# Optimization experiments

Measured on AMD Instinct MI355X. Metric: run time of the kernel, lower is better.

## Reference

```python
import jax, jax.numpy as jnp
import numpy as np

N_NODES = 50000
N_EDGES = 800000
HID = 128


def setup_inputs() -> dict:
    key = jax.random.key(0)
    ks = jax.random.split(key, 8)
    h = jax.random.normal(ks[0], (N_NODES, HID), dtype=jnp.float32)
    edge_index = jax.random.randint(ks[1], (2, N_EDGES), 0, N_NODES, dtype=jnp.int64)
    edge_attr = jax.random.normal(ks[2], (N_EDGES, HID), dtype=jnp.float32)
    # MLP params: Linear(3H -> H), Linear(H -> 1). Stored as [in, out] so y = x @ W + b.
    s1 = 1.0 / np.sqrt(3 * HID)
    W1 = jax.random.uniform(ks[3], (3 * HID, HID), minval=-s1, maxval=s1, dtype=jnp.float32)
    b1 = jax.random.uniform(ks[4], (HID,), minval=-s1, maxval=s1, dtype=jnp.float32)
    s2 = 1.0 / np.sqrt(HID)
    W2 = jax.random.uniform(ks[5], (HID, 1), minval=-s2, maxval=s2, dtype=jnp.float32)
    b2 = jax.random.uniform(ks[6], (1,), minval=-s2, maxval=s2, dtype=jnp.float32)
    return {"h": h, "edge_index": edge_index, "edge_attr": edge_attr,
            "W1": W1, "b1": b1, "W2": W2, "b2": b2}


def reference(h, edge_index, edge_attr, W1, b1, W2, b2):
    row, col = edge_index[0], edge_index[1]
    h_i = h[row]                      # [E, H] gather of source nodes
    h_j = h[col]                      # [E, H] gather of target nodes
    # Split first Linear over the concat [h_i, h_j, edge_attr] to avoid a [E, 3H] buffer.
    Wa, Wb, Wc = W1[:HID], W1[HID:2 * HID], W1[2 * HID:]
    pre = h_i @ Wa + h_j @ Wb + edge_attr @ Wc + b1      # [E, H]
    a = jax.nn.elu(pre) @ W2 + b2                        # [E, 1]
    a = jax.nn.leaky_relu(a, negative_slope=0.2)
    alpha = jax.nn.softmax(a, axis=0)                    # softmax over all edges (dim=0)
    h_agg = jnp.zeros_like(h).at[row].add(alpha * h_j)   # scatter-add weighted neighbors
    return h_agg
```

## Files before the change

### kernel.cpp

```cpp
#include <hip/hip_runtime.h>
#include <hip/hip_bf16.h>
#include <math.h>

#define NNODES 50000
#define NEDGES 800000
#define HID    128
#define NB_SCAN 196
#define NB_EDGE 6250

typedef short bf16x8 __attribute__((ext_vector_type(8)));
typedef float f32x4  __attribute__((ext_vector_type(4)));

__device__ __forceinline__ unsigned short bf16_rn(float x) {
    union { float f; unsigned int u; } v; v.f = x;
    unsigned int r = v.u + 0x7fffu + ((v.u >> 16) & 1u);
    return (unsigned short)(r >> 16);
}
__device__ __forceinline__ float bf16_to_f(unsigned short u) {
    union { unsigned int u; float f; } v; v.u = ((unsigned int)u) << 16;
    return v.f;
}

__device__ __forceinline__ float expm1_fast(float x) {
    float t = 1.9841270e-4f;
    t = fmaf(t, x, 1.3888889e-3f);
    t = fmaf(t, x, 8.3333333e-3f);
    t = fmaf(t, x, 4.1666668e-2f);
    t = fmaf(t, x, 0.16666667f);
    t = fmaf(t, x, 0.5f);
    t = fmaf(t, x, 1.0f);
    float poly = x * t;
    float ex   = __expf(x) - 1.0f;
    return (x > -0.25f) ? poly : ex;
}

__global__ void k_prep(const float* __restrict__ W1, unsigned short* __restrict__ Wt,
                       unsigned short* __restrict__ WH, unsigned short* __restrict__ WL)
{
    int t = blockIdx.x * 256 + threadIdx.x;
    const float* Wc = W1 + 256 * 128;
#pragma unroll
    for (int i = t * 4; i < t * 4 + 4; ++i) {
        int c = i >> 7, k = i & 127;
        Wt[c * 128 + k] = bf16_rn(Wc[k * 128 + c]);
    }
#pragma unroll
    for (int i = t * 8; i < t * 8 + 8; ++i) {
        int half = i >> 14, c = (i >> 7) & 127, k = i & 127;
        float v = W1[(half * 128 + k) * 128 + c];
        unsigned short hi = bf16_rn(v);
        float res = v - bf16_to_f(hi);
        WH[i] = hi;
        WL[i] = bf16_rn(res);
    }
}

__global__ __launch_bounds__(256) void k_gemm_mfma(
    const float* __restrict__ h, const unsigned short* __restrict__ WH,
    const unsigned short* __restrict__ WL, const float* __restrict__ b1,
    unsigned short* __restrict__ Hab)
{
    const int tid  = threadIdx.x;
    const int w    = tid >> 6;
    const int l    = tid & 63;
    const int quad = l >> 4;
    const int lm   = l & 15;
    const int wm   = w * 32;
    const int nb   = blockIdx.x * 128;
    const int by   = blockIdx.y;
    const unsigned short* __restrict__ BH = WH + by * 16384;
    const unsigned short* __restrict__ BL = WL + by * 16384;

    const int node0 = nb + wm + lm;
    const int node1 = node0 + 16;
    const bool v0 = node0 < NNODES, v1 = node1 < NNODES;
    const float* a0 = h + (size_t)node0 * 128 + quad * 8;
    const float* a1 = h + (size_t)node1 * 128 + quad * 8;
    const float4 fz = make_float4(0.f, 0.f, 0.f, 0.f);

    f32x4 acc[2][8] = {};
    float4 raw[2][2][2];
    raw[0][0][0] = v0 ? *(const float4*)(a0)     : fz;
    raw[0][0][1] = v0 ? *(const float4*)(a0 + 4) : fz;
    raw[0][1][0] = v1 ? *(const float4*)(a1)     : fz;
    raw[0][1][1] = v1 ? *(const float4*)(a1 + 4) : fz;

#pragma unroll
    for (int stage = 0; stage < 4; ++stage) {
        const int ks  = stage * 32;
        const int cur = stage & 1, nxt = cur ^ 1;
        if (stage < 3) {
            const int ko = ks + 32;
            raw[nxt][0][0] = v0 ? *(const float4*)(a0 + ko)     : fz;
            raw[nxt][0][1] = v0 ? *(const float4*)(a0 + ko + 4) : fz;
            raw[nxt][1][0] = v1 ? *(const float4*)(a1 + ko)     : fz;
            raw[nxt][1][1] = v1 ? *(const float4*)(a1 + ko + 4) : fz;
        }
        bf16x8 bh[8], bl[8];
#pragma unroll
        for (int nt = 0; nt < 8; ++nt) {
            const int c = lm * 8 + nt;
            bh[nt] = *(const bf16x8*)(BH + c * 128 + ks + quad * 8);
            bl[nt] = *(const bf16x8*)(BL + c * 128 + ks + quad * 8);
        }
        bf16x8 ahh[2], ahl[2];
#pragma unroll
        for (int mt = 0; mt < 2; ++mt) {
            float x[8];
            *(float4*)&x[0] = raw[cur][mt][0];
            *(float4*)&x[4] = raw[cur][mt][1];
            bf16x8 fh, fl;
#pragma unroll
            for (int j = 0; j < 8; ++j) {
                unsigned short hi = bf16_rn(x[j]);
                float res = x[j] - bf16_to_f(hi);
                fh[j] = (short)hi;
                fl[j] = (short)bf16_rn(res);
            }
            ahh[mt] = fh; ahl[mt] = fl;
        }
#pragma unroll
        for (int mt = 0; mt < 2; ++mt)
#pragma unroll
            for (int nt = 0; nt < 8; ++nt) {
                acc[mt][nt] = __builtin_amdgcn_mfma_f32_16x16x32_bf16(
                    ahh[mt], bh[nt], acc[mt][nt], 0, 0, 0);
                acc[mt][nt] = __builtin_amdgcn_mfma_f32_16x16x32_bf16(
                    ahh[mt], bl[nt], acc[mt][nt], 0, 0, 0);
                acc[mt][nt] = __builtin_amdgcn_mfma_f32_16x16x32_bf16(
                    ahl[mt], bh[nt], acc[mt][nt], 0, 0, 0);
            }
    }

    float b1v[8];
    if (by == 0) {
        *(float4*)&b1v[0] = *(const float4*)&b1[lm * 8];
        *(float4*)&b1v[4] = *(const float4*)&b1[lm * 8 + 4];
    } else {
#pragma unroll
        for (int c = 0; c < 8; ++c) b1v[c] = 0.f;
    }
#pragma unroll
    for (int mt = 0; mt < 2; ++mt) {
#pragma unroll
        for (int r = 0; r < 4; ++r) {
            int node = nb + wm + mt * 16 + quad * 4 + r;
            if (node < NNODES) {
                unsigned short o[8];
#pragma unroll
                for (int nt = 0; nt < 8; ++nt)
                    o[nt] = bf16_rn(acc[mt][nt][r] + b1v[nt]);
                *(int4*)(Hab + (size_t)node * 256 + by * 128 + lm * 8) = *(int4*)&o[0];
            }
        }
    }
}

__global__ __launch_bounds__(256) void k_edge_mfma(
    const float* __restrict__ ea, const int* __restrict__ eidx,
    const unsigned short* __restrict__ Wt, const float* __restrict__ W2,
    const float* __restrict__ b2, const unsigned short* __restrict__ Hab,
    float* __restrict__ a_out, int* __restrict__ hist,
    float* __restrict__ bmax, float* __restrict__ bsumE)
{
    const int tid  = threadIdx.x;
    const int w    = tid >> 6;
    const int l    = tid & 63;
    const int quad = l >> 4;
    const int lm   = l & 15;
    const int wm   = w * 32;
    const int ebase = blockIdx.x * 128;

    __shared__ __align__(16) unsigned short wlds[16384];
    __shared__ float sred[8];

#pragma unroll
    for (int i = 0; i < 8; ++i) {
        int idx16 = i * 2048 + tid * 8;
        int c = idx16 >> 7;
        bf16x8 v = *(const bf16x8*)(Wt + idx16);
        int byte = (idx16 * 2) ^ (((c >> 3) & 15) << 4);
        *(bf16x8*)((char*)wlds + byte) = v;
    }
    __syncthreads();

    int rows0[4], cols0[4], rows1[4], cols1[4];
    const int e40 = ebase + wm + quad * 4;
    {
        int4 r0 = *(const int4*)(eidx + e40);
        int4 c0 = *(const int4*)(eidx + NEDGES + e40);
        int4 r1 = *(const int4*)(eidx + e40 + 16);
        int4 c1 = *(const int4*)(eidx + NEDGES + e40 + 16);
        rows0[0] = r0.x; rows0[1] = r0.y; rows0[2] = r0.z; rows0[3] = r0.w;
        cols0[0] = c0.x; cols0[1] = c0.y; cols0[2] = c0.z; cols0[3] = c0.w;
        rows1[0] = r1.x; rows1[1] = r1.y; rows1[2] = r1.z; rows1[3] = r1.w;
        cols1[0] = c1.x; cols1[1] = c1.y; cols1[2] = c1.z; cols1[3] = c1.w;
    }

    const float* abase0 = ea + (size_t)(ebase + wm + lm) * 128 + quad * 8;
    const float* abase1 = abase0 + 16 * 128;
    float4 raw[2][2][2];
    raw[0][0][0] = *(const float4*)(abase0);
    raw[0][0][1] = *(const float4*)(abase0 + 4);
    raw[0][1][0] = *(const float4*)(abase1);
    raw[0][1][1] = *(const float4*)(abase1 + 4);

    bf16x8 hav[2][4], hbv[2][4];
#pragma unroll
    for (int r = 0; r < 4; ++r) {
        hav[0][r] = *(const bf16x8*)(Hab + (size_t)rows0[r] * 256 + lm * 8);
        hbv[0][r] = *(const bf16x8*)(Hab + (size_t)cols0[r] * 256 + 128 + lm * 8);
        hav[1][r] = *(const bf16x8*)(Hab + (size_t)rows1[r] * 256 + lm * 8);
        hbv[1][r] = *(const bf16x8*)(Hab + (size_t)cols1[r] * 256 + 128 + lm * 8);
    }
    asm volatile("" ::: "memory");

    f32x4 acc[2][8] = {};

#pragma unroll
    for (int stage = 0; stage < 4; ++stage) {
        const int ks  = stage * 32;
        const int cur = stage & 1, nxt = cur ^ 1;
        if (stage < 3) {
            const int ko = ks + 32;
            raw[nxt][0][0] = *(const float4*)(abase0 + ko);
            raw[nxt][0][1] = *(const float4*)(abase0 + ko + 4);
            raw[nxt][1][0] = *(const float4*)(abase1 + ko);
            raw[nxt][1][1] = *(const float4*)(abase1 + ko + 4);
        }
        bf16x8 bfrag[8];
#pragma unroll
        for (int nt = 0; nt < 8; ++nt) {
            const int c = lm * 8 + nt;
            const int byte = (c * 256 + (ks + quad * 8) * 2) ^ ((lm & 15) << 4);
            bfrag[nt] = *(const bf16x8*)((const char*)wlds + byte);
        }
        bf16x8 afrag[2];
#pragma unroll
        for (int mt = 0; mt < 2; ++mt) {
            float4 x0 = raw[cur][mt][0];
            float4 x1 = raw[cur][mt][1];
            bf16x8 f;
            f[0] = (short)bf16_rn(x0.x); f[1] = (short)bf16_rn(x0.y);
            f[2] = (short)bf16_rn(x0.z); f[3] = (short)bf16_rn(x0.w);
            f[4] = (short)bf16_rn(x1.x); f[5] = (short)bf16_rn(x1.y);
            f[6] = (short)bf16_rn(x1.z); f[7] = (short)bf16_rn(x1.w);
            afrag[mt] = f;
        }
#pragma unroll
        for (int mt = 0; mt < 2; ++mt)
#pragma unroll
            for (int nt = 0; nt < 8; ++nt)
                acc[mt][nt] = __builtin_amdgcn_mfma_f32_16x16x32_bf16(
                    afrag[mt], bfrag[nt], acc[mt][nt], 0, 0, 0);
    }

    float w2v[8];
    *(float4*)&w2v[0] = *(const float4*)&W2[lm * 8];
    *(float4*)&w2v[4] = *(const float4*)&W2[lm * 8 + 4];
    const float b2s = b2[0];

    float avl[2] = { -INFINITY, -INFINITY };

#pragma unroll
    for (int mt = 0; mt < 2; ++mt) {
        const int e4 = ebase + wm + mt * 16 + quad * 4;

        float s0 = 0.f, s1 = 0.f, s2 = 0.f, s3 = 0.f;
#pragma unroll
        for (int r = 0; r < 4; ++r) {
            float sr = 0.f;
#pragma unroll
            for (int nt = 0; nt < 8; ++nt) {
                float ha  = bf16_to_f((unsigned short)hav[mt][r][nt]);
                float hb  = bf16_to_f((unsigned short)hbv[mt][r][nt]);
                float pre = acc[mt][nt][r] + ha + hb;
                float el  = pre > 0.f ? pre : expm1_fast(pre);
                sr = fmaf(el, w2v[nt], sr);
            }
            if (r == 0) s0 = sr; else if (r == 1) s1 = sr; else if (r == 2) s2 = sr; else s3 = sr;
        }
#pragma unroll
        for (int m = 1; m < 16; m <<= 1) {
            s0 += __shfl_xor(s0, m, 64);
            s1 += __shfl_xor(s1, m, 64);
            s2 += __shfl_xor(s2, m, 64);
            s3 += __shfl_xor(s3, m, 64);
        }
        if (lm < 4) {
            float sum = (lm == 0) ? s0 : (lm == 1) ? s1 : (lm == 2) ? s2 : s3;
            sum += b2s;
            float av = sum >= 0.f ? sum : 0.2f * sum;
            a_out[e4 + lm] = av;
            avl[mt] = av;
        }
    }

    float m = fmaxf(avl[0], avl[1]);
#pragma unroll
    for (int msk = 1; msk < 64; msk <<= 1) m = fmaxf(m, __shfl_xor(m, msk, 64));
    if (l == 0) sred[w] = m;
    __syncthreads();
    float mb = fmaxf(fmaxf(sred[0], sred[1]), fmaxf(sred[2], sred[3]));
    float es = 0.f;
    if (avl[0] > -INFINITY)
        es = expf(avl[0] - mb) + expf(avl[1] - mb);
#pragma unroll
    for (int msk = 1; msk < 64; msk <<= 1) es += __shfl_xor(es, msk, 64);
    if (l == 0) sred[4 + w] = es;
    __syncthreads();
    if (tid == 0) {
        bmax[blockIdx.x]  = mb;
        bsumE[blockIdx.x] = sred[4] + sred[5] + sred[6] + sred[7];
    }

    if (lm == 0) {
#pragma unroll
        for (int r = 0; r < 4; ++r) {
            atomicAdd(&hist[rows0[r]], 1);
            atomicAdd(&hist[rows1[r]], 1);
        }
    }
}

__global__ void k_scan_blk(const int* __restrict__ hist, int* __restrict__ offsets,
                           int* __restrict__ bsum)
{
    __shared__ int sd[256];
    int t = threadIdx.x, i = blockIdx.x * 256 + t;
    int v = (i < NNODES) ? hist[i] : 0;
    sd[t] = v; __syncthreads();
    for (int off = 1; off < 256; off <<= 1) {
        int add = (t >= off) ? sd[t - off] : 0;
        __syncthreads();
        sd[t] += add;
        __syncthreads();
    }
    if (i < NNODES) offsets[i] = sd[t] - v;
    if (t == 255) bsum[blockIdx.x] = sd[255];
}

__global__ void k_scan_top(const int* __restrict__ bsum, int* __restrict__ bpre,
                           int* __restrict__ offsets)
{
    __shared__ int sd[256];
    int t = threadIdx.x;
    int v = (t < NB_SCAN) ? bsum[t] : 0;
    sd[t] = v; __syncthreads();
    for (int off = 1; off < 256; off <<= 1) {
        int add = (t >= off) ? sd[t - off] : 0;
        __syncthreads();
        sd[t] += add;
        __syncthreads();
    }
    if (t < NB_SCAN) bpre[t] = sd[t] - v;
    if (t == 255) offsets[NNODES] = sd[255];
}

__global__ void k_scan_add(int* __restrict__ offsets, const int* __restrict__ bpre)
{
    int i = blockIdx.x * 256 + threadIdx.x;
    if (i < NNODES) offsets[i] += bpre[i >> 8];
}

__global__ __launch_bounds__(1024) void k_final(
    const float* __restrict__ bmax, const float* __restrict__ bsumE,
    float* __restrict__ mz)
{
    __shared__ float sd[1024];
    int tid = threadIdx.x;
    float m = -INFINITY;
    for (int i = tid; i < NB_EDGE; i += 1024) m = fmaxf(m, bmax[i]);
    sd[tid] = m; __syncthreads();
    for (int off = 512; off > 0; off >>= 1) {
        if (tid < off) sd[tid] = fmaxf(sd[tid], sd[tid + off]);
        __syncthreads();
    }
    float M = sd[0];
    __syncthreads();
    float s = 0.f;
    for (int i = tid; i < NB_EDGE; i += 1024) s += bsumE[i] * expf(bmax[i] - M);
    sd[tid] = s; __syncthreads();
    for (int off = 512; off > 0; off >>= 1) {
        if (tid < off) sd[tid] += sd[tid + off];
        __syncthreads();
    }
    if (tid == 0) { mz[0] = M; mz[1] = 1.0f / sd[0]; }
}

__global__ void k_scatter(const int* __restrict__ eidx, const int* __restrict__ offsets,
                          int* __restrict__ cursor, const float* __restrict__ a,
                          const float* __restrict__ mz, int2* __restrict__ pairs)
{
    int e = blockIdx.x * 256 + threadIdx.x;
    if (e < NEDGES) {
        int r    = eidx[e];
        float al = expf(a[e] - mz[0]) * mz[1];
        int pos  = offsets[r] + atomicAdd(&cursor[r], 1);
        pairs[pos] = make_int2(__float_as_int(al), eidx[NEDGES + e]);
    }
}

__global__ __launch_bounds__(256) void k_agg(
    const float* __restrict__ h, const int2* __restrict__ pairs,
    const int* __restrict__ offsets, float* __restrict__ out)
{
    int node = blockIdx.x * 4 + (threadIdx.x >> 6);
    int lane = threadIdx.x & 63;
    if (node >= NNODES) return;
    int s0 = offsets[node], s1 = offsets[node + 1];
    float2 acc = make_float2(0.0f, 0.0f);
    int i = s0;
    for (; i + 8 <= s1; i += 8) {
        int2 p[8];
#pragma unroll
        for (int r = 0; r < 8; ++r) p[r] = pairs[i + r];
        float2 hv[8];
#pragma unroll
        for (int r = 0; r < 8; ++r)
            hv[r] = *(const float2*)(h + (size_t)p[r].y * 128 + lane * 2);
#pragma unroll
        for (int r = 0; r < 8; ++r) {
            float al = __int_as_float(p[r].x);
            acc.x = fmaf(al, hv[r].x, acc.x);
            acc.y = fmaf(al, hv[r].y, acc.y);
        }
    }
    for (; i < s1; ++i) {
        int2 p = pairs[i];
        float al = __int_as_float(p.x);
        float2 hj = *(const float2*)(h + (size_t)p.y * 128 + lane * 2);
        acc.x = fmaf(al, hj.x, acc.x);
        acc.y = fmaf(al, hj.y, acc.y);
    }
    *(float2*)(out + (size_t)node * 128 + lane * 2) = acc;
}

extern "C" void kernel_launch(void* const* d_in, const int* in_sizes, int n_in,
                              void* d_out, int out_size, void* d_ws, size_t ws_size,
                              hipStream_t stream)
{
    const float* h    = (const float*)d_in[0];
    const int*   eidx = (const int*)d_in[1];
    const float* ea   = (const float*)d_in[2];
    const float* W1   = (const float*)d_in[3];
    const float* b1   = (const float*)d_in[4];
    const float* W2   = (const float*)d_in[5];
    const float* b2   = (const float*)d_in[6];
    float* out = (float*)d_out;

    char* ws = (char*)d_ws;
    unsigned short* Hab = (unsigned short*)(ws);
    float* a_arr   = (float*)(ws + 25600000);
    int2*  pairs   = (int2*) (ws + 28800000);
    int*   offsets = (int*)  (ws + 35200000);
    float* bmax    = (float*)(ws + 35600384);
    float* bsumE   = (float*)(ws + 35625984);
    float* mz      = (float*)(ws + 35651584);
    unsigned short* Wt = (unsigned short*)(ws + 35651648);
    int*   bsum_s  = (int*)  (ws + 35684416);
    int*   bpre_s  = (int*)  (ws + 35685440);
    int*   cursorA = (int*)  (ws + 35686464);
    int*   cursorB = (int*)  (ws + 35886464);
    unsigned short* WH = (unsigned short*)(ws + 36086464);
    unsigned short* WL = (unsigned short*)(ws + 36152000);

    hipMemsetAsync(cursorA, 0, 400000, stream);

    k_prep<<<16, 256, 0, stream>>>(W1, Wt, WH, WL);
    k_gemm_mfma<<<dim3((NNODES + 127) / 128, 2), 256, 0, stream>>>(h, WH, WL, b1, Hab);

    k_edge_mfma<<<NB_EDGE, 256, 0, stream>>>(ea, eidx, Wt, W2, b2, Hab,
                                             a_arr, cursorA, bmax, bsumE);

    k_scan_blk<<<NB_SCAN, 256, 0, stream>>>(cursorA, offsets, bsum_s);
    k_scan_top<<<1, 256, 0, stream>>>(bsum_s, bpre_s, offsets);
    k_scan_add<<<NB_SCAN, 256, 0, stream>>>(offsets, bpre_s);

    k_final<<<1, 1024, 0, stream>>>(bmax, bsumE, mz);
    k_scatter<<<(NEDGES + 255) / 256, 256, 0, stream>>>(eidx, offsets, cursorB,
                                                        a_arr, mz, pairs);
    k_agg<<<(NNODES + 3) / 4, 256, 0, stream>>>(h, pairs, offsets, out);
}
```

Measured before the change: 807.4 us.

## Merge scan and softmax-final kernels; reorder edge-kernel loads around LDS staging

The three-kernel histogram scan and the global softmax reduction are merged into one two-block launch. Block 0 does a chunked single-block exclusive scan over the histogram while block 1 reduces the per-block max and sum, which removes three launches and their dependency gaps. In the edge kernel, the histogram atomics now issue before the LDS barrier and the node-feature gathers move into the last stage of the K loop. This is meant to overlap latency with the weight staging, but the gathers may now stall the final stage instead. The single-block serial scan over 49-element chunks per thread has less parallelism than the old multi-block scan.

```diff
diff --git a/kernel.cpp b/kernel.cpp
--- a/kernel.cpp
+++ b/kernel.cpp
@@ -5,7 +5,6 @@
 #define NNODES 50000
 #define NEDGES 800000
 #define HID    128
-#define NB_SCAN 196
 #define NB_EDGE 6250
 
 typedef short bf16x8 __attribute__((ext_vector_type(8)));
@@ -182,11 +181,12 @@
         int byte = (idx16 * 2) ^ (((c >> 3) & 15) << 4);
         *(bf16x8*)((char*)wlds + byte) = v;
     }
-    __syncthreads();
+
+    f32x4 acc[2][8] = {};
 
     int rows0[4], cols0[4], rows1[4], cols1[4];
-    const int e40 = ebase + wm + quad * 4;
     {
+        const int e40 = ebase + wm + quad * 4;
         int4 r0 = *(const int4*)(eidx + e40);
         int4 c0 = *(const int4*)(eidx + NEDGES + e40);
         int4 r1 = *(const int4*)(eidx + e40 + 16);
@@ -196,6 +196,13 @@
         rows1[0] = r1.x; rows1[1] = r1.y; rows1[2] = r1.z; rows1[3] = r1.w;
         cols1[0] = c1.x; cols1[1] = c1.y; cols1[2] = c1.z; cols1[3] = c1.w;
     }
+    if (lm == 0) {
+#pragma unroll
+        for (int r = 0; r < 4; ++r) {
+            atomicAdd(&hist[rows0[r]], 1);
+            atomicAdd(&hist[rows1[r]], 1);
+        }
+    }
 
     const float* abase0 = ea + (size_t)(ebase + wm + lm) * 128 + quad * 8;
     const float* abase1 = abase0 + 16 * 128;
@@ -206,16 +213,8 @@
     raw[0][1][1] = *(const float4*)(abase1 + 4);
 
     bf16x8 hav[2][4], hbv[2][4];
-#pragma unroll
-    for (int r = 0; r < 4; ++r) {
-        hav[0][r] = *(const bf16x8*)(Hab + (size_t)rows0[r] * 256 + lm * 8);
-        hbv[0][r] = *(const bf16x8*)(Hab + (size_t)cols0[r] * 256 + 128 + lm * 8);
-        hav[1][r] = *(const bf16x8*)(Hab + (size_t)rows1[r] * 256 + lm * 8);
-        hbv[1][r] = *(const bf16x8*)(Hab + (size_t)cols1[r] * 256 + 128 + lm * 8);
-    }
-    asm volatile("" ::: "memory");
-
-    f32x4 acc[2][8] = {};
+
+    __syncthreads();
 
 #pragma unroll
     for (int stage = 0; stage < 4; ++stage) {
@@ -228,6 +227,15 @@
             raw[nxt][1][0] = *(const float4*)(abase1 + ko);
             raw[nxt][1][1] = *(const float4*)(abase1 + ko + 4);
         }
+        if (stage == 3) {
+#pragma unroll
+            for (int r = 0; r < 4; ++r) {
+                hav[0][r] = *(const bf16x8*)(Hab + (size_t)rows0[r] * 256 + lm * 8);
+                hbv[0][r] = *(const bf16x8*)(Hab + (size_t)cols0[r] * 256 + 128 + lm * 8);
+                hav[1][r] = *(const bf16x8*)(Hab + (size_t)rows1[r] * 256 + lm * 8);
+                hbv[1][r] = *(const bf16x8*)(Hab + (size_t)cols1[r] * 256 + 128 + lm * 8);
+            }
+        }
         bf16x8 bfrag[8];
 #pragma unroll
         for (int nt = 0; nt < 8; ++nt) {
@@ -313,79 +321,60 @@
         bmax[blockIdx.x]  = mb;
         bsumE[blockIdx.x] = sred[4] + sred[5] + sred[6] + sred[7];
     }
-
-    if (lm == 0) {
-#pragma unroll
-        for (int r = 0; r < 4; ++r) {
-            atomicAdd(&hist[rows0[r]], 1);
-            atomicAdd(&hist[rows1[r]], 1);
-        }
-    }
-}
-
-__global__ void k_scan_blk(const int* __restrict__ hist, int* __restrict__ offsets,
-                           int* __restrict__ bsum)
-{
-    __shared__ int sd[256];
-    int t = threadIdx.x, i = blockIdx.x * 256 + t;
-    int v = (i < NNODES) ? hist[i] : 0;
-    sd[t] = v; __syncthreads();
-    for (int off = 1; off < 256; off <<= 1) {
-        int add = (t >= off) ? sd[t - off] : 0;
-        __syncthreads();
-        sd[t] += add;
-        __syncthreads();
-    }
-    if (i < NNODES) offsets[i] = sd[t] - v;
-    if (t == 255) bsum[blockIdx.x] = sd[255];
-}
-
-__global__ void k_scan_top(const int* __restrict__ bsum, int* __restrict__ bpre,
-                           int* __restrict__ offsets)
-{
-    __shared__ int sd[256];
-    int t = threadIdx.x;
-    int v = (t < NB_SCAN) ? bsum[t] : 0;
-    sd[t] = v; __syncthreads();
-    for (int off = 1; off < 256; off <<= 1) {
-        int add = (t >= off) ? sd[t - off] : 0;
-        __syncthreads();
-        sd[t] += add;
-        __syncthreads();
-    }
-    if (t < NB_SCAN) bpre[t] = sd[t] - v;
-    if (t == 255) offsets[NNODES] = sd[255];
-}
-
-__global__ void k_scan_add(int* __restrict__ offsets, const int* __restrict__ bpre)
-{
-    int i = blockIdx.x * 256 + threadIdx.x;
-    if (i < NNODES) offsets[i] += bpre[i >> 8];
-}
-
-__global__ __launch_bounds__(1024) void k_final(
+}
+
+__global__ __launch_bounds__(1024) void k_scan_final(
+    const int* __restrict__ hist, int* __restrict__ offsets,
     const float* __restrict__ bmax, const float* __restrict__ bsumE,
     float* __restrict__ mz)
 {
+    __shared__ int   part[1024];
     __shared__ float sd[1024];
-    int tid = threadIdx.x;
-    float m = -INFINITY;
-    for (int i = tid; i < NB_EDGE; i += 1024) m = fmaxf(m, bmax[i]);
-    sd[tid] = m; __syncthreads();
-    for (int off = 512; off > 0; off >>= 1) {
-        if (tid < off) sd[tid] = fmaxf(sd[tid], sd[tid + off]);
+    const int t = threadIdx.x;
+
+    if (blockIdx.x == 0) {
+        const int CH = 49;
+        const int base = t * CH;
+        int s = 0;
+        for (int i = 0; i < CH; ++i) {
+            int idx = base + i;
+            s += (idx < NNODES) ? hist[idx] : 0;
+        }
+        part[t] = s; __syncthreads();
+        for (int off = 1; off < 1024; off <<= 1) {
+            int add = (t >= off) ? part[t - off] : 0;
+            __syncthreads();
+            part[t] += add;
+            __syncthreads();
+        }
+        int run = (t == 0) ? 0 : part[t - 1];
+        for (int i = 0; i < CH; ++i) {
+            int idx = base + i;
+            if (idx < NNODES) {
+                offsets[idx] = run;
+                run += hist[idx];
+            }
+        }
+        if (t == 1023) offsets[NNODES] = part[1023];
+    } else {
+        float m = -INFINITY;
+        for (int i = t; i < NB_EDGE; i += 1024) m = fmaxf(m, bmax[i]);
+        sd[t] = m; __syncthreads();
+        for (int off = 512; off > 0; off >>= 1) {
+            if (t < off) sd[t] = fmaxf(sd[t], sd[t + off]);
+            __syncthreads();
+        }
+        float M = sd[0];
         __syncthreads();
-    }
-    float M = sd[0];
-    __syncthreads();
-    float s = 0.f;
-    for (int i = tid; i < NB_EDGE; i += 1024) s += bsumE[i] * expf(bmax[i] - M);
-    sd[tid] = s; __syncthreads();
-    for (int off = 512; off > 0; off >>= 1) {
-        if (tid < off) sd[tid] += sd[tid + off];
-        __syncthreads();
-    }
-    if (tid == 0) { mz[0] = M; mz[1] = 1.0f / sd[0]; }
+        float s = 0.f;
+        for (int i = t; i < NB_EDGE; i += 1024) s += bsumE[i] * expf(bmax[i] - M);
+        sd[t] = s; __syncthreads();
+        for (int off = 512; off > 0; off >>= 1) {
+            if (t < off) sd[t] += sd[t + off];
+            __syncthreads();
+        }
+        if (t == 0) { mz[0] = M; mz[1] = 1.0f / sd[0]; }
+    }
 }
 
 __global__ void k_scatter(const int* __restrict__ eidx, const int* __restrict__ offsets,
@@ -458,8 +447,6 @@
     float* bsumE   = (float*)(ws + 35625984);
     float* mz      = (float*)(ws + 35651584);
     unsigned short* Wt = (unsigned short*)(ws + 35651648);
-    int*   bsum_s  = (int*)  (ws + 35684416);
-    int*   bpre_s  = (int*)  (ws + 35685440);
     int*   cursorA = (int*)  (ws + 35686464);
     int*   cursorB = (int*)  (ws + 35886464);
     unsigned short* WH = (unsigned short*)(ws + 36086464);
@@ -473,11 +460,8 @@
     k_edge_mfma<<<NB_EDGE, 256, 0, stream>>>(ea, eidx, Wt, W2, b2, Hab,
                                              a_arr, cursorA, bmax, bsumE);
 
-    k_scan_blk<<<NB_SCAN, 256, 0, stream>>>(cursorA, offsets, bsum_s);
-    k_scan_top<<<1, 256, 0, stream>>>(bsum_s, bpre_s, offsets);
-    k_scan_add<<<NB_SCAN, 256, 0, stream>>>(offsets, bpre_s);
-
-    k_final<<<1, 1024, 0, stream>>>(bmax, bsumE, mz);
+    k_scan_final<<<2, 1024, 0, stream>>>(cursorA, offsets, bmax, bsumE, mz);
+
     k_scatter<<<(NEDGES + 255) / 256, 256, 0, stream>>>(eidx, offsets, cursorB,
                                                         a_arr, mz, pairs);
     k_agg<<<(NNODES + 3) / 4, 256, 0, stream>>>(h, pairs, offsets, out);
```

Measured after the change: 859.6 us. +6.5%, slower.

## Replace CSR scan and scatter with fixed-capacity per-node buckets filled in edge kernel

Applied to the files above, without the earlier changes.

The edge kernel now appends each edge's (score, col) pair straight into a fixed 64-slot per-node bucket through an atomic counter, with a small global overflow list. This removes the histogram, the three scan kernels, the scatter kernel and the intermediate score array. The softmax exp and normalisation move into the aggregation kernel. The Hab gather loads are also deferred to the last MFMA stage to shorten register live ranges. The risks are more per-edge atomics inside the edge kernel, sparse bucket memory reads, and a linear overflow scan in every aggregation warp if any node has more than 64 edges. Overflow beyond 4096 entries would be silently dropped.

```diff
diff --git a/kernel.cpp b/kernel.cpp
--- a/kernel.cpp
+++ b/kernel.cpp
@@ -5,8 +5,9 @@
 #define NNODES 50000
 #define NEDGES 800000
 #define HID    128
-#define NB_SCAN 196
 #define NB_EDGE 6250
+#define BCAP   64
+#define OVFCAP 4096
 
 typedef short bf16x8 __attribute__((ext_vector_type(8)));
 typedef float f32x4  __attribute__((ext_vector_type(4)));
@@ -160,7 +161,8 @@
     const float* __restrict__ ea, const int* __restrict__ eidx,
     const unsigned short* __restrict__ Wt, const float* __restrict__ W2,
     const float* __restrict__ b2, const unsigned short* __restrict__ Hab,
-    float* __restrict__ a_out, int* __restrict__ hist,
+    int* __restrict__ cnt, int2* __restrict__ bucket,
+    int* __restrict__ ovf_cnt, int4* __restrict__ ovf,
     float* __restrict__ bmax, float* __restrict__ bsumE)
 {
     const int tid  = threadIdx.x;
@@ -182,11 +184,12 @@
         int byte = (idx16 * 2) ^ (((c >> 3) & 15) << 4);
         *(bf16x8*)((char*)wlds + byte) = v;
     }
-    __syncthreads();
+
+    f32x4 acc[2][8] = {};
 
     int rows0[4], cols0[4], rows1[4], cols1[4];
-    const int e40 = ebase + wm + quad * 4;
     {
+        const int e40 = ebase + wm + quad * 4;
         int4 r0 = *(const int4*)(eidx + e40);
         int4 c0 = *(const int4*)(eidx + NEDGES + e40);
         int4 r1 = *(const int4*)(eidx + e40 + 16);
@@ -206,16 +209,8 @@
     raw[0][1][1] = *(const float4*)(abase1 + 4);
 
     bf16x8 hav[2][4], hbv[2][4];
-#pragma unroll
-    for (int r = 0; r < 4; ++r) {
-        hav[0][r] = *(const bf16x8*)(Hab + (size_t)rows0[r] * 256 + lm * 8);
-        hbv[0][r] = *(const bf16x8*)(Hab + (size_t)cols0[r] * 256 + 128 + lm * 8);
-        hav[1][r] = *(const bf16x8*)(Hab + (size_t)rows1[r] * 256 + lm * 8);
-        hbv[1][r] = *(const bf16x8*)(Hab + (size_t)cols1[r] * 256 + 128 + lm * 8);
-    }
-    asm volatile("" ::: "memory");
-
-    f32x4 acc[2][8] = {};
+
+    __syncthreads();
 
 #pragma unroll
     for (int stage = 0; stage < 4; ++stage) {
@@ -228,6 +223,15 @@
             raw[nxt][1][0] = *(const float4*)(abase1 + ko);
             raw[nxt][1][1] = *(const float4*)(abase1 + ko + 4);
         }
+        if (stage == 3) {
+#pragma unroll
+            for (int r = 0; r < 4; ++r) {
+                hav[0][r] = *(const bf16x8*)(Hab + (size_t)rows0[r] * 256 + lm * 8);
+                hbv[0][r] = *(const bf16x8*)(Hab + (size_t)cols0[r] * 256 + 128 + lm * 8);
+                hav[1][r] = *(const bf16x8*)(Hab + (size_t)rows1[r] * 256 + lm * 8);
+                hbv[1][r] = *(const bf16x8*)(Hab + (size_t)cols1[r] * 256 + 128 + lm * 8);
+            }
+        }
         bf16x8 bfrag[8];
 #pragma unroll
         for (int nt = 0; nt < 8; ++nt) {
@@ -264,8 +268,6 @@
 
 #pragma unroll
     for (int mt = 0; mt < 2; ++mt) {
-        const int e4 = ebase + wm + mt * 16 + quad * 4;
-
         float s0 = 0.f, s1 = 0.f, s2 = 0.f, s3 = 0.f;
 #pragma unroll
         for (int r = 0; r < 4; ++r) {
@@ -291,7 +293,21 @@
             float sum = (lm == 0) ? s0 : (lm == 1) ? s1 : (lm == 2) ? s2 : s3;
             sum += b2s;
             float av = sum >= 0.f ? sum : 0.2f * sum;
-            a_out[e4 + lm] = av;
+            int row, col;
+            if (mt == 0) {
+                row = (lm == 0) ? rows0[0] : (lm == 1) ? rows0[1] : (lm == 2) ? rows0[2] : rows0[3];
+                col = (lm == 0) ? cols0[0] : (lm == 1) ? cols0[1] : (lm == 2) ? cols0[2] : cols0[3];
+            } else {
+                row = (lm == 0) ? rows1[0] : (lm == 1) ? rows1[1] : (lm == 2) ? rows1[2] : rows1[3];
+                col = (lm == 0) ? cols1[0] : (lm == 1) ? cols1[1] : (lm == 2) ? cols1[2] : cols1[3];
+            }
+            int pos = atomicAdd(&cnt[row], 1);
+            if (pos < BCAP) {
+                bucket[(size_t)row * BCAP + pos] = make_int2(__float_as_int(av), col);
+            } else {
+                int o = atomicAdd(ovf_cnt, 1);
+                if (o < OVFCAP) ovf[o] = make_int4(row, __float_as_int(av), col, 0);
+            }
             avl[mt] = av;
         }
     }
@@ -313,54 +329,6 @@
         bmax[blockIdx.x]  = mb;
         bsumE[blockIdx.x] = sred[4] + sred[5] + sred[6] + sred[7];
     }
-
-    if (lm == 0) {
-#pragma unroll
-        for (int r = 0; r < 4; ++r) {
-            atomicAdd(&hist[rows0[r]], 1);
-            atomicAdd(&hist[rows1[r]], 1);
-        }
-    }
-}
-
-__global__ void k_scan_blk(const int* __restrict__ hist, int* __restrict__ offsets,
-                           int* __restrict__ bsum)
-{
-    __shared__ int sd[256];
-    int t = threadIdx.x, i = blockIdx.x * 256 + t;
-    int v = (i < NNODES) ? hist[i] : 0;
-    sd[t] = v; __syncthreads();
-    for (int off = 1; off < 256; off <<= 1) {
-        int add = (t >= off) ? sd[t - off] : 0;
-        __syncthreads();
-        sd[t] += add;
-        __syncthreads();
-    }
-    if (i < NNODES) offsets[i] = sd[t] - v;
-    if (t == 255) bsum[blockIdx.x] = sd[255];
-}
-
-__global__ void k_scan_top(const int* __restrict__ bsum, int* __restrict__ bpre,
-                           int* __restrict__ offsets)
-{
-    __shared__ int sd[256];
-    int t = threadIdx.x;
-    int v = (t < NB_SCAN) ? bsum[t] : 0;
-    sd[t] = v; __syncthreads();
-    for (int off = 1; off < 256; off <<= 1) {
-        int add = (t >= off) ? sd[t - off] : 0;
-        __syncthreads();
-        sd[t] += add;
-        __syncthreads();
-    }
-    if (t < NB_SCAN) bpre[t] = sd[t] - v;
-    if (t == 255) offsets[NNODES] = sd[255];
-}
-
-__global__ void k_scan_add(int* __restrict__ offsets, const int* __restrict__ bpre)
-{
-    int i = blockIdx.x * 256 + threadIdx.x;
-    if (i < NNODES) offsets[i] += bpre[i >> 8];
 }
 
 __global__ __launch_bounds__(1024) void k_final(
@@ -388,50 +356,57 @@
     if (tid == 0) { mz[0] = M; mz[1] = 1.0f / sd[0]; }
 }
 
-__global__ void k_scatter(const int* __restrict__ eidx, const int* __restrict__ offsets,
-                          int* __restrict__ cursor, const float* __restrict__ a,
-                          const float* __restrict__ mz, int2* __restrict__ pairs)
-{
-    int e = blockIdx.x * 256 + threadIdx.x;
-    if (e < NEDGES) {
-        int r    = eidx[e];
-        float al = expf(a[e] - mz[0]) * mz[1];
-        int pos  = offsets[r] + atomicAdd(&cursor[r], 1);
-        pairs[pos] = make_int2(__float_as_int(al), eidx[NEDGES + e]);
-    }
-}
-
 __global__ __launch_bounds__(256) void k_agg(
-    const float* __restrict__ h, const int2* __restrict__ pairs,
-    const int* __restrict__ offsets, float* __restrict__ out)
+    const float* __restrict__ h, const int2* __restrict__ bucket,
+    const int* __restrict__ cnt, const int* __restrict__ ovf_cnt,
+    const int4* __restrict__ ovf, const float* __restrict__ mz,
+    float* __restrict__ out)
 {
     int node = blockIdx.x * 4 + (threadIdx.x >> 6);
     int lane = threadIdx.x & 63;
     if (node >= NNODES) return;
-    int s0 = offsets[node], s1 = offsets[node + 1];
+    const float M    = mz[0];
+    const float invS = mz[1];
+    int degT = cnt[node];
+    int deg  = degT < BCAP ? degT : BCAP;
+    const int2* bk = bucket + (size_t)node * BCAP;
+
     float2 acc = make_float2(0.0f, 0.0f);
-    int i = s0;
-    for (; i + 8 <= s1; i += 8) {
+    int i = 0;
+    for (; i + 8 <= deg; i += 8) {
         int2 p[8];
 #pragma unroll
-        for (int r = 0; r < 8; ++r) p[r] = pairs[i + r];
+        for (int r = 0; r < 8; ++r) p[r] = bk[i + r];
         float2 hv[8];
 #pragma unroll
         for (int r = 0; r < 8; ++r)
             hv[r] = *(const float2*)(h + (size_t)p[r].y * 128 + lane * 2);
 #pragma unroll
         for (int r = 0; r < 8; ++r) {
-            float al = __int_as_float(p[r].x);
+            float al = expf(__int_as_float(p[r].x) - M) * invS;
             acc.x = fmaf(al, hv[r].x, acc.x);
             acc.y = fmaf(al, hv[r].y, acc.y);
         }
     }
-    for (; i < s1; ++i) {
-        int2 p = pairs[i];
-        float al = __int_as_float(p.x);
+    for (; i < deg; ++i) {
+        int2 p = bk[i];
+        float al = expf(__int_as_float(p.x) - M) * invS;
         float2 hj = *(const float2*)(h + (size_t)p.y * 128 + lane * 2);
         acc.x = fmaf(al, hj.x, acc.x);
         acc.y = fmaf(al, hj.y, acc.y);
+    }
+    int oc = *ovf_cnt;
+    if (oc > 0) {
+        if (oc > OVFCAP) oc = OVFCAP;
+        for (int o = 0; o < oc; ++o) {
+            int4 e = ovf[o];
+            if (e.x == node) {
+                float al = expf(__int_as_float(e.y) - M) * invS;
+                float2 hj = *(const float2*)(h + (size_t)e.z * 128 + lane * 2);
+                acc.x = fmaf(al, hj.x, acc.x);
+                acc.y = fmaf(al, hj.y, acc.y);
+            }
+        }
     }
     *(float2*)(out + (size_t)node * 128 + lane * 2) = acc;
 }
@@ -451,34 +426,25 @@
 
     char* ws = (char*)d_ws;
     unsigned short* Hab = (unsigned short*)(ws);
-    float* a_arr   = (float*)(ws + 25600000);
-    int2*  pairs   = (int2*) (ws + 28800000);
-    int*   offsets = (int*)  (ws + 35200000);
-    float* bmax    = (float*)(ws + 35600384);
-    float* bsumE   = (float*)(ws + 35625984);
-    float* mz      = (float*)(ws + 35651584);
-    unsigned short* Wt = (unsigned short*)(ws + 35651648);
-    int*   bsum_s  = (int*)  (ws + 35684416);
-    int*   bpre_s  = (int*)  (ws + 35685440);
-    int*   cursorA = (int*)  (ws + 35686464);
-    int*   cursorB = (int*)  (ws + 35886464);
-    unsigned short* WH = (unsigned short*)(ws + 36086464);
-    unsigned short* WL = (unsigned short*)(ws + 36152000);
-
-    hipMemsetAsync(cursorA, 0, 400000, stream);
+    int2*  bucket = (int2*) (ws + 25600000);
+    int*   cnt    = (int*)  (ws + 51200000);
+    int*   ovfc   = (int*)  (ws + 51400000);
+    int4*  ovf    = (int4*) (ws + 51400064);
+    float* bmax   = (float*)(ws + 51465600);
+    float* bsumE  = (float*)(ws + 51491200);
+    float* mz     = (float*)(ws + 51516800);
+    unsigned short* Wt = (unsigned short*)(ws + 51516864);
+    unsigned short* WH = (unsigned short*)(ws + 51549632);
+    unsigned short* WL = (unsigned short*)(ws + 51615168);
+
+    hipMemsetAsync(cnt, 0, 200064, stream);
 
     k_prep<<<16, 256, 0, stream>>>(W1, Wt, WH, WL);
     k_gemm_mfma<<<dim3((NNODES + 127) / 128, 2), 256, 0, stream>>>(h, WH, WL, b1, Hab);
 
     k_edge_mfma<<<NB_EDGE, 256, 0, stream>>>(ea, eidx, Wt, W2, b2, Hab,
-                                             a_arr, cursorA, bmax, bsumE);
-
-    k_scan_blk<<<NB_SCAN, 256, 0, stream>>>(cursorA, offsets, bsum_s);
-    k_scan_top<<<1, 256, 0, stream>>>(bsum_s, bpre_s, offsets);
-    k_scan_add<<<NB_SCAN, 256, 0, stream>>>(offsets, bpre_s);
+                                             cnt, bucket, ovfc, ovf, bmax, bsumE);
 
     k_final<<<1, 1024, 0, stream>>>(bmax, bsumE, mz);
-    k_scatter<<<(NEDGES + 255) / 256, 256, 0, stream>>>(eidx, offsets, cursorB,
-                                                        a_arr, mz, pairs);
-    k_agg<<<(NNODES + 3) / 4, 256, 0, stream>>>(h, pairs, offsets, out);
-}
+    k_agg<<<(NNODES + 3) / 4, 256, 0, stream>>>(h, bucket, cnt, ovfc, ovf, mz, out);
+}
```

After: 752.6 us. 6.8% less time.
